# Performance work log

Measured on AMD Instinct MI355X. Metric: run time of the kernel, lower is better.

## Reference

```python
import jax, jax.numpy as jnp
import numpy as np
from jax import lax

B = 4096          # number of utterance nodes
D_IN = 1856       # 512 audio + 512 visual + 768 text + 64 speaker
H = 128           # hidden_dim
N_STEPS = 4       # fixed-step RK4 steps over t in [0, 1]
ALPHA1, ALPHA2, BETA = 0.8, 0.5, 0.1


def setup_inputs() -> dict:
    key = jax.random.key(0)
    ks = jax.random.split(key, 10)
    features = jax.random.normal(ks[0], (B, D_IN), dtype=jnp.float32)
    speaker_ids = jax.random.randint(ks[1], (B,), 0, 12)
    modality_masks = jax.random.uniform(ks[2], (B, 3), dtype=jnp.float32)
    # params stored as [in, out]; y = x @ W + b (matches torch Linear math)
    s_in = 1.0 / np.sqrt(D_IN)
    Wp = jax.random.uniform(ks[3], (D_IN, H), minval=-s_in, maxval=s_in, dtype=jnp.float32)
    bp = jax.random.uniform(ks[4], (H,), minval=-s_in, maxval=s_in, dtype=jnp.float32)
    s1 = 1.0 / np.sqrt(2 * H)
    W1 = jax.random.uniform(ks[5], (2 * H, H), minval=-s1, maxval=s1, dtype=jnp.float32)
    b1 = jax.random.uniform(ks[6], (H,), minval=-s1, maxval=s1, dtype=jnp.float32)
    s2 = 1.0 / np.sqrt(H)
    W2 = jax.random.uniform(ks[7], (H, H), minval=-s2, maxval=s2, dtype=jnp.float32)
    b2 = jax.random.uniform(ks[8], (H,), minval=-s2, maxval=s2, dtype=jnp.float32)
    return {"features": features, "speaker_ids": speaker_ids,
            "modality_masks": modality_masks, "Wp": Wp, "bp": bp,
            "W1": W1, "b1": b1, "W2": W2, "b2": b2}


def build_graph(speaker_ids, modality_masks):
    idx = jnp.arange(B)
    time_diff = jnp.abs(idx[:, None] - idx[None, :]).astype(jnp.float32)  # [B,B]
    temporal = jnp.exp(-BETA * time_diff)
    same_spk = speaker_ids[:, None] == speaker_ids[None, :]
    # mean_c |m_i,c - m_j,c| without materializing [B,B,3]
    mod_diff = sum(jnp.abs(modality_masks[:, c][:, None] - modality_masks[:, c][None, :])
                   for c in range(3)) * (1.0 / 3.0)
    mod_sim = 1.0 - mod_diff
    off_diag = jnp.where(same_spk, ALPHA1 * temporal, ALPHA2 * temporal * mod_sim)
    adj = jnp.where(idx[:, None] == idx[None, :], 1.0, off_diag)
    adj = adj / (adj.sum(axis=-1, keepdims=True) + 1e-8)
    return adj


def reference(features, speaker_ids, modality_masks, Wp, bp, W1, b1, W2, b2):
    h0 = features @ Wp + bp                      # [B,H] input projection
    adj = build_graph(speaker_ids, modality_masks)

    def ode_func(h):
        h_neighbors = adj @ h                    # [B,H] neighbor aggregation
        h_combined = jnp.concatenate([h, h_neighbors], axis=-1)  # [B,2H]
        return jnp.tanh(h_combined @ W1 + b1) @ W2 + b2

    dt = 1.0 / N_STEPS

    def rk4_step(h, _):
        k1 = ode_func(h)
        k2 = ode_func(h + 0.5 * dt * k1)
        k3 = ode_func(h + 0.5 * dt * k2)
        k4 = ode_func(h + dt * k3)
        return h + (dt / 6.0) * (k1 + 2.0 * k2 + 2.0 * k3 + k4), None

    h_final, _ = lax.scan(rk4_step, h0, None, length=N_STEPS)
    return h_final
```

## Files before the change

kernel.cpp:

```cpp
#include <hip/hip_runtime.h>


typedef unsigned short u16;
typedef unsigned long long u64;
typedef __attribute__((ext_vector_type(8))) short bf16x8v;
typedef __attribute__((ext_vector_type(4))) float f32x4;

#define MFMA16(a, b, c) __builtin_amdgcn_mfma_f32_16x16x32_bf16(a, b, c, 0, 0, 0)

#define BN 4096
#define HN 128
#define DIN 1856
#define TILEW 320
#define IBSTRIDE 32

__device__ __forceinline__ float bf2f(u16 u) {
  union { unsigned u; float f; } v; v.u = ((unsigned)u) << 16; return v.f;
}
__device__ __forceinline__ u16 f2bf(float f) {
  union { float f; unsigned u; } v; v.f = f;
  unsigned u = v.u;
  return (u16)((u + 0x7fffu + ((u >> 16) & 1u)) >> 16);
}
__device__ __forceinline__ float ldx(const void* p, long idx, int isf) {
  return isf ? ((const float*)p)[idx] : bf2f(((const u16*)p)[idx]);
}
__device__ __forceinline__ int ldspk(const void* spk, int j, int i64) {
  return i64 ? ((const int*)spk)[2 * j] : ((const int*)spk)[j];
}

__device__ __forceinline__ void cstore8(u16* p, u64 v) {
  __hip_atomic_store((u64*)p, v, __ATOMIC_RELAXED, __HIP_MEMORY_SCOPE_AGENT);
}

__global__ __launch_bounds__(256) void detect(
    const void* a0, const void* a1, const void* a2, const void* a3,
    const void* a4, const void* a5, const void* a6, const void* a7,
    const unsigned* spk_raw, int* flags, int* inbox) {
  __shared__ int part[256];
  const int b = blockIdx.x, t = threadIdx.x;
  int cnt = 0;
  if (b < 8) {
    const void* arr[8] = {a0, a1, a2, a3, a4, a5, a6, a7};
    const int nel[8] = {BN * DIN, BN * 3, DIN * HN, HN, 2 * HN * HN, HN, HN * HN, HN};
    const u16* p = (const u16*)arr[b];
    int ns = nel[b] / 2; if (ns > 512) ns = 512;
    for (int e = t; e < ns; e += 256) {
      unsigned ex = (p[2 * e] >> 7) & 0xFFu;
      if (ex < 64u) cnt++;
    }
  } else if (b == 8) {
    for (int e = t; e < 512; e += 256)
      if (spk_raw[2 * e + 1] != 0u) cnt++;
  } else {
    inbox[t * IBSTRIDE] = 0;
    return;
  }
  part[t] = cnt;
  __syncthreads();
  #pragma unroll
  for (int o = 128; o > 0; o >>= 1) {
    if (t < o) part[t] += part[t + o];
    __syncthreads();
  }
  if (t == 0) {
    if (b < 8) flags[b] = (part[0] >= 2) ? 1 : 0;
    else       flags[9] = (part[0] == 0) ? 1 : 0;
  }
}

__device__ __forceinline__ float adjr(int i, int j, int si, float m0, float m1, float m2,
                                      const void* __restrict__ spk,
                                      const void* __restrict__ mk, int fm, int fs) {
  if (i == j) return 1.0f;
  float t = expf(-0.1f * fabsf((float)(i - j)));
  if (ldspk(spk, j, fs) == si) return 0.8f * t;
  float ms = fabsf(m0 - ldx(mk, (long)j * 3, fm)) +
             fabsf(m1 - ldx(mk, (long)j * 3 + 1, fm)) +
             fabsf(m2 - ldx(mk, (long)j * 3 + 2, fm));
  return 0.5f * t * (1.0f - ms * (1.0f / 3.0f));
}

#define FEATBLK 3712
#define NWBLK 1120
__global__ __launch_bounds__(256) void prep(
    const void* feat, const void* Wp, const void* W1, const void* W2,
    const void* masks, const void* spk,
    const void* x0, const void* x1, const void* x2,
    const int* __restrict__ flags,
    u16* featc, u16* WpT, u16* W1T, u16* W2T,
    float* bp_c, float* b1c, float* b2c, u16* __restrict__ band) {
  __shared__ float part[256];
  __shared__ float invs;
  __shared__ float mxs[3][64];
  __shared__ int ord[3];
  const int blk = blockIdx.x, t = threadIdx.x;
  if (blk < FEATBLK) {
    if (!flags[0]) return;
    long e = ((long)blk * 256 + t) * 8;
    const float* pf = (const float*)feat + e;
    u16 r[8];
    #pragma unroll
    for (int k = 0; k < 8; k++) r[k] = f2bf(pf[k]);
    *(bf16x8v*)(featc + e) = *(bf16x8v*)r;
    return;
  }
  if (blk < FEATBLK + NWBLK) {
    long e = (long)(blk - FEATBLK) * 256 + t;
    const int nWp = DIN * HN, nW1 = 2 * HN * HN;
    if (e < nWp) {
      int k = e >> 7, o = e & 127;
      WpT[(long)o * DIN + k] = f2bf(ldx(Wp, e, flags[2]));
      return;
    }
    e -= nWp;
    if (e < nW1) { int k = e >> 7, o = e & 127; W1T[(long)o * 256 + k] = f2bf(ldx(W1, e, flags[4])); return; }
    e -= nW1;
    { int k = e >> 7, o = e & 127; W2T[(long)o * 128 + k] = f2bf(ldx(W2, e, flags[6])); }
    return;
  }
  if (blk == FEATBLK + NWBLK) {
    const void* bs[3] = {x0, x1, x2};
    const int fl[3] = {flags[3], flags[5], flags[7]};
    if (t < 192) {
      int a = t / 64, e = t % 64;
      mxs[a][e] = fmaxf(fabsf(ldx(bs[a], e, fl[a])), fabsf(ldx(bs[a], e + 64, fl[a])));
    }
    __syncthreads();
    if (t == 0) {
      float mx[3];
      for (int a = 0; a < 3; a++) {
        float m = 0.f;
        for (int e = 0; e < 64; e++) m = fmaxf(m, mxs[a][e]);
        mx[a] = m;
      }
      int imin = 0, imax = 0;
      for (int k = 1; k < 3; k++) { if (mx[k] < mx[imin]) imin = k; if (mx[k] > mx[imax]) imax = k; }
      int imid = 3 - imin - imax;
      if (imin == imax) { imin = 0; imid = 1; imax = 2; }
      ord[0] = imin; ord[1] = imid; ord[2] = imax;
    }
    __syncthreads();
    if (t < HN) {
      bp_c[t] = ldx(bs[ord[0]], t, fl[ord[0]]);
      b1c[t]  = ldx(bs[ord[1]], t, fl[ord[1]]);
      b2c[t]  = ldx(bs[ord[2]], t, fl[ord[2]]);
    }
    return;
  }
  {
    const int i = blk - FEATBLK - NWBLK - 1;
    const int fm = flags[1], fs = flags[9];
    const int si = ldspk(spk, i, fs);
    const float m0 = ldx(masks, (long)i * 3, fm);
    const float m1 = ldx(masks, (long)i * 3 + 1, fm);
    const float m2 = ldx(masks, (long)i * 3 + 2, fm);
    float s = 0.f;
    for (int j = t; j < BN; j += 256) s += adjr(i, j, si, m0, m1, m2, spk, masks, fm, fs);
    part[t] = s;
    __syncthreads();
    if (t == 0) {
      float tot = 0.f;
      for (int k = 0; k < 256; k++) tot += part[k];
      invs = 1.0f / (tot + 1e-8f);
    }
    __syncthreads();
    const float inv = invs;
    const int jbase = (i & ~15) - 128;
    for (int k = t; k < TILEW; k += 256) {
      int j = jbase + k;
      float v = 0.f;
      if (j >= 0 && j < BN) v = adjr(i, j, si, m0, m1, m2, spk, masks, fm, fs) * inv;
      band[(long)i * TILEW + k] = f2bf(v);
    }
  }
}

#define SNAP_ELEMS ((size_t)HN * BN + 8192)

__global__ __launch_bounds__(512, 2) void fused_ode(
    const void* __restrict__ feat, const int* __restrict__ flags,
    const u16* __restrict__ featc, const u16* __restrict__ WpT,
    const float* __restrict__ bp_c, const u16* __restrict__ band,
    const u16* __restrict__ W1T, const u16* __restrict__ W2T,
    const float* __restrict__ b1c, const float* __restrict__ b2c,
    u16* __restrict__ hsb, float* __restrict__ outp,
    int* __restrict__ inbox) {
  __shared__ u16 hc[16][264];
  __shared__ u16 zt[16][136];

  const int tid = threadIdx.x, w = tid >> 6, lane = tid & 63;
  const int m = lane & 15, q = lane >> 4;
  const int blk = blockIdx.x;
  const int tile = ((blk & 7) << 5) | (blk >> 3);
  const int r0 = tile * 16, jb = r0 - 128;
  const int n0 = w * 16 + m;
  const int i0 = r0 + q * 4;
  const long base = (long)n0 * BN + i0;

  const int plo = (tile - 8 < 0) ? 0 : tile - 8;
  const int phi = (tile + 11 > 255) ? 255 : tile + 11;
  const int nprod = phi - plo + 1;
  const int cons = tile - 11 + tid;
  const int cvalid = (tid < 20) && (cons >= 0) && (cons < 256);

  bf16x8v w1r[8], w2r[4], bnd[10];
  {
    const u16* w1row = W1T + (long)n0 * 256;
    #pragma unroll
    for (int kf = 0; kf < 8; kf++) {
      int k = (kf >> 1) * 64 + (kf & 1) * 32 + q * 8;
      w1r[kf] = *(const bf16x8v*)(w1row + k);
    }
    const u16* w2row = W2T + (long)n0 * 128;
    #pragma unroll
    for (int kf = 0; kf < 4; kf++) {
      int k = (kf >> 1) * 64 + (kf & 1) * 32 + q * 8;
      w2r[kf] = *(const bf16x8v*)(w2row + k);
    }
    const u16* bandrow = band + (long)tile * 5120 + m * TILEW;
    #pragma unroll
    for (int kf = 0; kf < 10; kf++) {
      int k = (kf >> 1) * 64 + (kf & 1) * 32 + q * 8;
      bnd[kf] = *(const bf16x8v*)(bandrow + k);
    }
  }
  const float b1v = b1c[n0], b2v = b2c[n0];

  f32x4 hb;
  {
    const u16* fbase = flags[0] ? featc : (const u16*)feat;
    f32x4 a0 = {0, 0, 0, 0};
    const u16* arow = fbase + (long)(r0 + m) * DIN;
    const u16* brow = WpT + (long)n0 * DIN;
    #pragma unroll 4
    for (int kf = 0; kf < 58; kf++) {
      int k = (kf >> 1) * 64 + (kf & 1) * 32 + q * 8;
      bf16x8v a = *(const bf16x8v*)(arow + k);
      bf16x8v b = *(const bf16x8v*)(brow + k);
      a0 = MFMA16(a, b, a0);
    }
    a0 += bp_c[n0];
    hb = a0;
  }
  f32x4 acc = {0, 0, 0, 0};
  {
    u16* snap0 = hsb + 4096;
    ushort4 hsv;
    hsv.x = f2bf(hb[0]); hsv.y = f2bf(hb[1]); hsv.z = f2bf(hb[2]); hsv.w = f2bf(hb[3]);
    union { ushort4 s; u64 q8; } pu; pu.s = hsv;
    cstore8(&snap0[base], pu.q8);
    hc[q * 4 + 0][n0] = hsv.x; hc[q * 4 + 1][n0] = hsv.y;
    hc[q * 4 + 2][n0] = hsv.z; hc[q * 4 + 3][n0] = hsv.w;
  }
  asm volatile("s_waitcnt vmcnt(0)" ::: "memory");
  __syncthreads();
  if (cvalid)
    __hip_atomic_fetch_add(&inbox[cons * IBSTRIDE], 1, __ATOMIC_RELAXED,
                           __HIP_MEMORY_SCOPE_AGENT);

  const float dt6 = 0.25f / 6.0f;

  #pragma unroll 1
  for (int s = 0; s < 16; s++) {
    const int sub = s & 3;

    f32x4 z0 = {0, 0, 0, 0};
    #pragma unroll
    for (int kf = 0; kf < 4; kf++) {
      int k = (kf >> 1) * 64 + (kf & 1) * 32 + q * 8;
      bf16x8v a = *(const bf16x8v*)&hc[m][k];
      z0 = MFMA16(a, w1r[kf], z0);
    }

    if (tid == 0) {
      const int tgt = nprod * (s + 1);
      while (__hip_atomic_load(&inbox[tile * IBSTRIDE], __ATOMIC_RELAXED,
                               __HIP_MEMORY_SCOPE_AGENT) < tgt)
        __builtin_amdgcn_s_sleep(1);
    }
    __syncthreads();

    f32x4 g0 = {0, 0, 0, 0};
    const u16* hrow = hsb + (size_t)s * SNAP_ELEMS + 4096 + (long)n0 * BN + jb;
    #pragma unroll
    for (int kf = 0; kf < 10; kf++) {
      int k = (kf >> 1) * 64 + (kf & 1) * 32 + q * 8;
      bf16x8v b = *(const bf16x8v*)(hrow + k);
      g0 = MFMA16(bnd[kf], b, g0);
    }
    #pragma unroll
    for (int r = 0; r < 4; r++) hc[q * 4 + r][128 + n0] = f2bf(g0[r]);
    __syncthreads();

    #pragma unroll
    for (int kf = 4; kf < 8; kf++) {
      int k = (kf >> 1) * 64 + (kf & 1) * 32 + q * 8;
      bf16x8v a = *(const bf16x8v*)&hc[m][k];
      z0 = MFMA16(a, w1r[kf], z0);
    }
    #pragma unroll
    for (int r = 0; r < 4; r++) zt[q * 4 + r][n0] = f2bf(tanhf(z0[r] + b1v));
    __syncthreads();

    f32x4 k0 = {0, 0, 0, 0};
    #pragma unroll
    for (int kf = 0; kf < 4; kf++) {
      int k = (kf >> 1) * 64 + (kf & 1) * 32 + q * 8;
      bf16x8v a = *(const bf16x8v*)&zt[m][k];
      k0 = MFMA16(a, w2r[kf], k0);
    }
    f32x4 kv = k0;
    kv += b2v;

    f32x4 hn;
    if (sub == 0)      { acc = 1.f * kv;  hn = hb + 0.125f * kv; }
    else if (sub == 1) { acc += 2.f * kv; hn = hb + 0.125f * kv; }
    else if (sub == 2) { acc += 2.f * kv; hn = hb + 0.25f  * kv; }
    else {
      hn = hb + dt6 * (acc + kv);
      hb = hn;
      if (s == 15) {
        #pragma unroll
        for (int r = 0; r < 4; r++) outp[(long)(i0 + r) * HN + n0] = hn[r];
      }
    }

    if (s < 15) {
      u16* snapw = hsb + (size_t)(s + 1) * SNAP_ELEMS + 4096;
      ushort4 hsv;
      hsv.x = f2bf(hn[0]); hsv.y = f2bf(hn[1]); hsv.z = f2bf(hn[2]); hsv.w = f2bf(hn[3]);
      union { ushort4 s4; u64 q8; } pu; pu.s4 = hsv;
      cstore8(&snapw[base], pu.q8);
      hc[q * 4 + 0][n0] = hsv.x; hc[q * 4 + 1][n0] = hsv.y;
      hc[q * 4 + 2][n0] = hsv.z; hc[q * 4 + 3][n0] = hsv.w;
      asm volatile("s_waitcnt vmcnt(0)" ::: "memory");
      __syncthreads();
      if (cvalid)
        __hip_atomic_fetch_add(&inbox[cons * IBSTRIDE], 1, __ATOMIC_RELAXED,
                               __HIP_MEMORY_SCOPE_AGENT);
    }
  }
}

extern "C" void kernel_launch(void* const* d_in, const int* in_sizes, int n_in,
                              void* d_out, int out_size, void* d_ws, size_t ws_size,
                              hipStream_t stream) {
  const void* feat = nullptr; const void* spk = nullptr; const void* masks = nullptr;
  const void* Wp = nullptr; const void* W1 = nullptr; const void* W2 = nullptr;
  const void* bias[3] = {nullptr, nullptr, nullptr};
  int nb = 0;
  for (int k = 0; k < n_in; k++) {
    switch (in_sizes[k]) {
      case BN * DIN:    feat = d_in[k]; break;
      case BN:          spk = d_in[k]; break;
      case BN * 3:      masks = d_in[k]; break;
      case DIN * HN:    Wp = d_in[k]; break;
      case 2 * HN * HN: W1 = d_in[k]; break;
      case HN * HN:     W2 = d_in[k]; break;
      default:          if (in_sizes[k] == HN && nb < 3) bias[nb++] = d_in[k]; break;
    }
  }
  float* out = (float*)d_out;

  char* p = (char*)d_ws;
  int*   flags   = (int*)p;   p += 64;
  float* bp_c    = (float*)p; p += 512;
  float* b1c     = (float*)p; p += 512;
  float* b2c     = (float*)p; p += 512;
  int*   inbox   = (int*)p;   p += 256 * IBSTRIDE * 4;
  u16*   featc   = (u16*)p;   p += (size_t)BN * DIN * 2;
  u16*   WpT     = (u16*)p;   p += (size_t)HN * DIN * 2;
  u16*   W1T     = (u16*)p;   p += (size_t)HN * 256 * 2;
  u16*   W2T     = (u16*)p;   p += (size_t)HN * HN * 2;
  u16*   band    = (u16*)p;   p += (size_t)BN * TILEW * 2;
  u16*   hsb     = (u16*)p;   p += 16 * SNAP_ELEMS * 2;
  (void)ws_size; (void)out_size;

  detect<<<10, 256, 0, stream>>>(feat, masks, Wp, bias[0], W1, bias[1], W2, bias[2],
                                 (const unsigned*)spk, flags, inbox);
  prep<<<FEATBLK + NWBLK + 1 + BN, 256, 0, stream>>>(
      feat, Wp, W1, W2, masks, spk, bias[0], bias[1], bias[2], flags,
      featc, WpT, W1T, W2T, bp_c, b1c, b2c, band);

  fused_ode<<<dim3(BN / 16), dim3(512), 0, stream>>>(
      feat, flags, featc, WpT, bp_c, band, W1T, W2T, b1c, b2c,
      hsb, out, inbox);
}
```

Measured before the change: 225.5 us.

## Collapse each ODE tile block to a single wavefront covering all output columns

Each 16-row tile block now runs as one 64-lane wavefront instead of eight. The single wavefront loops over all eight 16-column output slices and keeps W1/W2 in LDS rather than per-wave registers. This drops most __syncthreads calls and cuts block-level coordination. In exchange each block does eight times the MFMA work serially, needs about 100KB of LDS, and leaves far fewer waves resident to hide memory latency, including on the spin-wait and the input projection.

```diff
diff --git a/kernel.cpp b/kernel.cpp
--- a/kernel.cpp
+++ b/kernel.cpp
@@ -178,7 +178,7 @@
 
 #define SNAP_ELEMS ((size_t)HN * BN + 8192)
 
-__global__ __launch_bounds__(512, 2) void fused_ode(
+__global__ __launch_bounds__(64, 1) void fused_ode(
     const void* __restrict__ feat, const int* __restrict__ flags,
     const u16* __restrict__ featc, const u16* __restrict__ WpT,
     const float* __restrict__ bp_c, const u16* __restrict__ band,
@@ -186,38 +186,36 @@
     const float* __restrict__ b1c, const float* __restrict__ b2c,
     u16* __restrict__ hsb, float* __restrict__ outp,
     int* __restrict__ inbox) {
+  __shared__ u16 w1l[128 * 264];
+  __shared__ u16 w2l[128 * 136];
   __shared__ u16 hc[16][264];
   __shared__ u16 zt[16][136];
 
-  const int tid = threadIdx.x, w = tid >> 6, lane = tid & 63;
+  const int lane = threadIdx.x;
   const int m = lane & 15, q = lane >> 4;
   const int blk = blockIdx.x;
   const int tile = ((blk & 7) << 5) | (blk >> 3);
   const int r0 = tile * 16, jb = r0 - 128;
-  const int n0 = w * 16 + m;
   const int i0 = r0 + q * 4;
-  const long base = (long)n0 * BN + i0;
 
   const int plo = (tile - 8 < 0) ? 0 : tile - 8;
   const int phi = (tile + 11 > 255) ? 255 : tile + 11;
   const int nprod = phi - plo + 1;
-  const int cons = tile - 11 + tid;
-  const int cvalid = (tid < 20) && (cons >= 0) && (cons < 256);
-
-  bf16x8v w1r[8], w2r[4], bnd[10];
+  const int cons = tile - 11 + lane;
+  const int cvalid = (lane < 20) && (cons >= 0) && (cons < 256);
+
+  for (int idx = lane; idx < 128 * 32; idx += 64) {
+    int row = idx >> 5, seg = (idx & 31) * 8;
+    *(bf16x8v*)&w1l[row * 264 + seg] = *(const bf16x8v*)(W1T + (long)row * 256 + seg);
+  }
+  for (int idx = lane; idx < 128 * 16; idx += 64) {
+    int row = idx >> 4, seg = (idx & 15) * 8;
+    *(bf16x8v*)&w2l[row * 136 + seg] = *(const bf16x8v*)(W2T + (long)row * 128 + seg);
+  }
+
+  const f32x4 zero4 = {0.f, 0.f, 0.f, 0.f};
+  bf16x8v bnd[10];
   {
-    const u16* w1row = W1T + (long)n0 * 256;
-    #pragma unroll
-    for (int kf = 0; kf < 8; kf++) {
-      int k = (kf >> 1) * 64 + (kf & 1) * 32 + q * 8;
-      w1r[kf] = *(const bf16x8v*)(w1row + k);
-    }
-    const u16* w2row = W2T + (long)n0 * 128;
-    #pragma unroll
-    for (int kf = 0; kf < 4; kf++) {
-      int k = (kf >> 1) * 64 + (kf & 1) * 32 + q * 8;
-      w2r[kf] = *(const bf16x8v*)(w2row + k);
-    }
     const u16* bandrow = band + (long)tile * 5120 + m * TILEW;
     #pragma unroll
     for (int kf = 0; kf < 10; kf++) {
@@ -225,36 +223,48 @@
       bnd[kf] = *(const bf16x8v*)(bandrow + k);
     }
   }
-  const float b1v = b1c[n0], b2v = b2c[n0];
-
-  f32x4 hb;
+  float b1v[8], b2v[8];
+  #pragma unroll
+  for (int nt = 0; nt < 8; nt++) { b1v[nt] = b1c[nt * 16 + m]; b2v[nt] = b2c[nt * 16 + m]; }
+
+  f32x4 hb[8];
   {
+    f32x4 a0[8];
+    #pragma unroll
+    for (int nt = 0; nt < 8; nt++) a0[nt] = zero4;
     const u16* fbase = flags[0] ? featc : (const u16*)feat;
-    f32x4 a0 = {0, 0, 0, 0};
     const u16* arow = fbase + (long)(r0 + m) * DIN;
-    const u16* brow = WpT + (long)n0 * DIN;
-    #pragma unroll 4
+    #pragma unroll 2
     for (int kf = 0; kf < 58; kf++) {
       int k = (kf >> 1) * 64 + (kf & 1) * 32 + q * 8;
       bf16x8v a = *(const bf16x8v*)(arow + k);
-      bf16x8v b = *(const bf16x8v*)(brow + k);
-      a0 = MFMA16(a, b, a0);
-    }
-    a0 += bp_c[n0];
-    hb = a0;
-  }
-  f32x4 acc = {0, 0, 0, 0};
+      #pragma unroll
+      for (int nt = 0; nt < 8; nt++) {
+        bf16x8v b = *(const bf16x8v*)(WpT + (long)(nt * 16 + m) * DIN + k);
+        a0[nt] = MFMA16(a, b, a0[nt]);
+      }
+    }
+    #pragma unroll
+    for (int nt = 0; nt < 8; nt++) { a0[nt] += bp_c[nt * 16 + m]; hb[nt] = a0[nt]; }
+  }
+  f32x4 acr[8];
+  #pragma unroll
+  for (int nt = 0; nt < 8; nt++) acr[nt] = zero4;
   {
     u16* snap0 = hsb + 4096;
-    ushort4 hsv;
-    hsv.x = f2bf(hb[0]); hsv.y = f2bf(hb[1]); hsv.z = f2bf(hb[2]); hsv.w = f2bf(hb[3]);
-    union { ushort4 s; u64 q8; } pu; pu.s = hsv;
-    cstore8(&snap0[base], pu.q8);
-    hc[q * 4 + 0][n0] = hsv.x; hc[q * 4 + 1][n0] = hsv.y;
-    hc[q * 4 + 2][n0] = hsv.z; hc[q * 4 + 3][n0] = hsv.w;
+    #pragma unroll
+    for (int nt = 0; nt < 8; nt++) {
+      const int n0 = nt * 16 + m;
+      ushort4 hsv;
+      hsv.x = f2bf(hb[nt][0]); hsv.y = f2bf(hb[nt][1]);
+      hsv.z = f2bf(hb[nt][2]); hsv.w = f2bf(hb[nt][3]);
+      union { ushort4 s4; u64 q8; } pu; pu.s4 = hsv;
+      cstore8(&snap0[(long)n0 * BN + i0], pu.q8);
+      hc[q * 4 + 0][n0] = hsv.x; hc[q * 4 + 1][n0] = hsv.y;
+      hc[q * 4 + 2][n0] = hsv.z; hc[q * 4 + 3][n0] = hsv.w;
+    }
   }
   asm volatile("s_waitcnt vmcnt(0)" ::: "memory");
-  __syncthreads();
   if (cvalid)
     __hip_atomic_fetch_add(&inbox[cons * IBSTRIDE], 1, __ATOMIC_RELAXED,
                            __HIP_MEMORY_SCOPE_AGENT);
@@ -265,77 +275,98 @@
   for (int s = 0; s < 16; s++) {
     const int sub = s & 3;
 
-    f32x4 z0 = {0, 0, 0, 0};
-    #pragma unroll
-    for (int kf = 0; kf < 4; kf++) {
-      int k = (kf >> 1) * 64 + (kf & 1) * 32 + q * 8;
-      bf16x8v a = *(const bf16x8v*)&hc[m][k];
-      z0 = MFMA16(a, w1r[kf], z0);
-    }
-
-    if (tid == 0) {
+    if (lane == 0) {
       const int tgt = nprod * (s + 1);
       while (__hip_atomic_load(&inbox[tile * IBSTRIDE], __ATOMIC_RELAXED,
                                __HIP_MEMORY_SCOPE_AGENT) < tgt)
         __builtin_amdgcn_s_sleep(1);
     }
-    __syncthreads();
-
-    f32x4 g0 = {0, 0, 0, 0};
-    const u16* hrow = hsb + (size_t)s * SNAP_ELEMS + 4096 + (long)n0 * BN + jb;
+    asm volatile("" ::: "memory");
+
+    f32x4 g[8];
+    #pragma unroll
+    for (int nt = 0; nt < 8; nt++) g[nt] = zero4;
+    const u16* snapr = hsb + (size_t)s * SNAP_ELEMS + 4096 + jb;
     #pragma unroll
     for (int kf = 0; kf < 10; kf++) {
       int k = (kf >> 1) * 64 + (kf & 1) * 32 + q * 8;
-      bf16x8v b = *(const bf16x8v*)(hrow + k);
-      g0 = MFMA16(bnd[kf], b, g0);
-    }
-    #pragma unroll
-    for (int r = 0; r < 4; r++) hc[q * 4 + r][128 + n0] = f2bf(g0[r]);
-    __syncthreads();
-
-    #pragma unroll
-    for (int kf = 4; kf < 8; kf++) {
+      #pragma unroll
+      for (int nt = 0; nt < 8; nt++) {
+        bf16x8v b = *(const bf16x8v*)(snapr + (long)(nt * 16 + m) * BN + k);
+        g[nt] = MFMA16(bnd[kf], b, g[nt]);
+      }
+    }
+    #pragma unroll
+    for (int nt = 0; nt < 8; nt++) {
+      const int n0 = nt * 16 + m;
+      #pragma unroll
+      for (int r = 0; r < 4; r++) hc[q * 4 + r][128 + n0] = f2bf(g[nt][r]);
+    }
+
+    f32x4 z[8];
+    #pragma unroll
+    for (int nt = 0; nt < 8; nt++) z[nt] = zero4;
+    #pragma unroll
+    for (int kf = 0; kf < 8; kf++) {
       int k = (kf >> 1) * 64 + (kf & 1) * 32 + q * 8;
       bf16x8v a = *(const bf16x8v*)&hc[m][k];
-      z0 = MFMA16(a, w1r[kf], z0);
-    }
-    #pragma unroll
-    for (int r = 0; r < 4; r++) zt[q * 4 + r][n0] = f2bf(tanhf(z0[r] + b1v));
-    __syncthreads();
-
-    f32x4 k0 = {0, 0, 0, 0};
+      #pragma unroll
+      for (int nt = 0; nt < 8; nt++) {
+        bf16x8v b = *(const bf16x8v*)&w1l[(nt * 16 + m) * 264 + k];
+        z[nt] = MFMA16(a, b, z[nt]);
+      }
+    }
+    #pragma unroll
+    for (int nt = 0; nt < 8; nt++) {
+      const int n0 = nt * 16 + m;
+      #pragma unroll
+      for (int r = 0; r < 4; r++) zt[q * 4 + r][n0] = f2bf(tanhf(z[nt][r] + b1v[nt]));
+    }
+
+    f32x4 kk[8];
+    #pragma unroll
+    for (int nt = 0; nt < 8; nt++) kk[nt] = zero4;
     #pragma unroll
     for (int kf = 0; kf < 4; kf++) {
       int k = (kf >> 1) * 64 + (kf & 1) * 32 + q * 8;
       bf16x8v a = *(const bf16x8v*)&zt[m][k];
-      k0 = MFMA16(a, w2r[kf], k0);
-    }
-    f32x4 kv = k0;
-    kv += b2v;
-
-    f32x4 hn;
-    if (sub == 0)      { acc = 1.f * kv;  hn = hb + 0.125f * kv; }
-    else if (sub == 1) { acc += 2.f * kv; hn = hb + 0.125f * kv; }
-    else if (sub == 2) { acc += 2.f * kv; hn = hb + 0.25f  * kv; }
-    else {
-      hn = hb + dt6 * (acc + kv);
-      hb = hn;
-      if (s == 15) {
-        #pragma unroll
-        for (int r = 0; r < 4; r++) outp[(long)(i0 + r) * HN + n0] = hn[r];
-      }
-    }
-
+      #pragma unroll
+      for (int nt = 0; nt < 8; nt++) {
+        bf16x8v b = *(const bf16x8v*)&w2l[(nt * 16 + m) * 136 + k];
+        kk[nt] = MFMA16(a, b, kk[nt]);
+      }
+    }
+
+    u16* snapw = hsb + (size_t)(s + 1) * SNAP_ELEMS + 4096;
+    #pragma unroll
+    for (int nt = 0; nt < 8; nt++) {
+      f32x4 kv = kk[nt];
+      kv += b2v[nt];
+      f32x4 hn;
+      if (sub == 0)      { acr[nt] = 1.f * kv;  hn = hb[nt] + 0.125f * kv; }
+      else if (sub == 1) { acr[nt] += 2.f * kv; hn = hb[nt] + 0.125f * kv; }
+      else if (sub == 2) { acr[nt] += 2.f * kv; hn = hb[nt] + 0.25f  * kv; }
+      else {
+        hn = hb[nt] + dt6 * (acr[nt] + kv);
+        hb[nt] = hn;
+        if (s == 15) {
+          #pragma unroll
+          for (int r = 0; r < 4; r++)
+            outp[(long)(i0 + r) * HN + nt * 16 + m] = hn[r];
+        }
+      }
+      if (s < 15) {
+        const int n0 = nt * 16 + m;
+        ushort4 hsv;
+        hsv.x = f2bf(hn[0]); hsv.y = f2bf(hn[1]); hsv.z = f2bf(hn[2]); hsv.w = f2bf(hn[3]);
+        union { ushort4 s4; u64 q8; } pu; pu.s4 = hsv;
+        cstore8(&snapw[(long)n0 * BN + i0], pu.q8);
+        hc[q * 4 + 0][n0] = hsv.x; hc[q * 4 + 1][n0] = hsv.y;
+        hc[q * 4 + 2][n0] = hsv.z; hc[q * 4 + 3][n0] = hsv.w;
+      }
+    }
     if (s < 15) {
-      u16* snapw = hsb + (size_t)(s + 1) * SNAP_ELEMS + 4096;
-      ushort4 hsv;
-      hsv.x = f2bf(hn[0]); hsv.y = f2bf(hn[1]); hsv.z = f2bf(hn[2]); hsv.w = f2bf(hn[3]);
-      union { ushort4 s4; u64 q8; } pu; pu.s4 = hsv;
-      cstore8(&snapw[base], pu.q8);
-      hc[q * 4 + 0][n0] = hsv.x; hc[q * 4 + 1][n0] = hsv.y;
-      hc[q * 4 + 2][n0] = hsv.z; hc[q * 4 + 3][n0] = hsv.w;
       asm volatile("s_waitcnt vmcnt(0)" ::: "memory");
-      __syncthreads();
       if (cvalid)
         __hip_atomic_fetch_add(&inbox[cons * IBSTRIDE], 1, __ATOMIC_RELAXED,
                                __HIP_MEMORY_SCOPE_AGENT);
@@ -383,7 +414,7 @@
       feat, Wp, W1, W2, masks, spk, bias[0], bias[1], bias[2], flags,
       featc, WpT, W1T, W2T, bp_c, b1c, b2c, band);
 
-  fused_ode<<<dim3(BN / 16), dim3(512), 0, stream>>>(
+  fused_ode<<<dim3(256), dim3(64), 0, stream>>>(
       feat, flags, featc, WpT, bp_c, band, W1T, W2T, b1c, b2c,
       hsb, out, inbox);
 }
```

Result: slower. 390.6 us (+73.2%).
